# Performance work log

Hardware: AMD Instinct MI355X
Metric: run time of the kernel (lower is better)

Reference implementation:

```python
import jax, jax.numpy as jnp
import numpy as np

D = 1024
D_PRE_HEAD = 128
H = 16
D_ROPE = D_PRE_HEAD // 2          # 64
DC_V = D_PRE_HEAD                 # 128
DC_KV = D_PRE_HEAD // 8           # 16
DC_Q = D // 4                     # 256
Q_HEAD_DIM = D_PRE_HEAD + D_ROPE  # 192
MEG_D = D_PRE_HEAD + DC_V         # 256
MAX_LEN = 8192
EPS = 1e-7


def rms_norm(x, w):
    x32 = x.astype(jnp.float32)
    var = jnp.mean(x32 * x32, axis=-1, keepdims=True)
    return w * (x32 * jax.lax.rsqrt(var + EPS)).astype(x.dtype)


def rope_cos_sin():
    inv_freq = 1.0 / (10000.0 ** (jnp.arange(0, D_ROPE, 2, dtype=jnp.float32) / D_ROPE))
    freqs = jnp.outer(jnp.arange(MAX_LEN, dtype=jnp.float32), inv_freq)
    emb = jnp.concatenate([freqs, freqs], axis=-1)  # [MAX_LEN, D_ROPE]
    return jnp.cos(emb), jnp.sin(emb)


def rope_reshape(x):
    # view(...,d//2,2).transpose(-1,-2).reshape == concat(even, odd) along last dim
    return jnp.concatenate([x[..., 0::2], x[..., 1::2]], axis=-1)


def rope_rotate(x):
    h = x.shape[-1] // 2
    return jnp.concatenate([-x[..., h:], x[..., :h]], axis=-1)


def setup_inputs() -> dict:
    key = jax.random.key(0)
    ks = jax.random.split(key, 12)
    B, SQ, SKV = 2, 2048, 2048
    s = 0.02
    return {
        "q_inputs": jax.random.normal(ks[0], (B, SQ, D), jnp.float32),
        "kv_input": jax.random.normal(ks[1], (B, SKV, D), jnp.float32),
        "q_pos_ids": jax.random.randint(ks[2], (B, SQ), 0, MAX_LEN),
        "kv_pos_ids": jax.random.randint(ks[3], (B, SKV), 0, MAX_LEN),
        # weights stored as [in, out] (torch Linear weight transposed)
        "Wq_down": jax.random.normal(ks[4], (D, DC_Q), jnp.float32) * s,
        "q_norm_w": jnp.ones((DC_Q,), jnp.float32),
        "Wq_up": jax.random.normal(ks[5], (DC_Q, H * Q_HEAD_DIM), jnp.float32) * s,
        "Wkv_down": jax.random.normal(ks[6], (D, DC_KV + D_ROPE), jnp.float32) * s,
        "kv_norm_w": jnp.ones((DC_KV,), jnp.float32),
        "Wkv_up": jax.random.normal(ks[7], (DC_KV, H * MEG_D), jnp.float32) * s,
        "Wout": jax.random.normal(ks[8], (H * DC_V, D), jnp.float32) * s,
    }


def reference(q_inputs, kv_input, q_pos_ids, kv_pos_ids,
              Wq_down, q_norm_w, Wq_up, Wkv_down, kv_norm_w, Wkv_up, Wout):
    B, SQ, _ = q_inputs.shape
    SKV = kv_input.shape[1]

    # query path: low-rank down -> RMSNorm -> up
    q = rms_norm(q_inputs @ Wq_down, q_norm_w) @ Wq_up
    q = q.reshape(B, SQ, H, Q_HEAD_DIM).transpose(0, 2, 1, 3)  # [B,H,SQ,192]
    q_nope, q_rope = q[..., :D_PRE_HEAD], q[..., D_PRE_HEAD:]

    # kv path: compressed latent + decoupled rope slice
    ckv_full = kv_input @ Wkv_down                              # [B,SKV,DC_KV+D_ROPE]
    c_kv, k_rope = ckv_full[..., :DC_KV], ckv_full[..., DC_KV:]
    c_kv = rms_norm(c_kv, kv_norm_w)
    kv = (c_kv @ Wkv_up).reshape(B, SKV, H, MEG_D).transpose(0, 2, 1, 3)
    k_nope, value = kv[..., :D_PRE_HEAD], kv[..., D_PRE_HEAD:]  # [B,H,SKV,128] each
    k_rope = k_rope[:, None, :, :]                              # [B,1,SKV,64]

    # RoPE with per-token position ids
    cos, sin = rope_cos_sin()
    q_cos, q_sin = cos[q_pos_ids][:, None], sin[q_pos_ids][:, None]   # [B,1,SQ,64]
    k_cos, k_sin = cos[kv_pos_ids][:, None], sin[kv_pos_ids][:, None]
    qr = rope_reshape(q_rope)
    kr = rope_reshape(k_rope)
    q_rope = qr * q_cos + rope_rotate(qr) * q_sin
    k_rope = kr * k_cos + rope_rotate(kr) * k_sin

    query = jnp.concatenate([q_nope, q_rope], axis=-1)                         # [B,H,SQ,192]
    key_t = jnp.concatenate([k_nope, jnp.broadcast_to(k_rope, (B, H, SKV, D_ROPE))], axis=-1)

    scale = 1.0 / jnp.sqrt(jnp.asarray(Q_HEAD_DIM, query.dtype))
    scores = jnp.einsum('bhqd,bhkd->bhqk', query, key_t) * scale
    attn = jax.nn.softmax(scores, axis=-1)
    out = jnp.einsum('bhqk,bhkd->bhqd', attn, value)                           # [B,H,SQ,128]
    out = out.transpose(0, 2, 1, 3).reshape(B, SQ, H * DC_V)
    return out @ Wout
```

## Files before the change

### kernel.cpp

```cpp
#include <hip/hip_runtime.h>

typedef unsigned short u16;
typedef unsigned int u32;
typedef u16 u16x4 __attribute__((ext_vector_type(4)));
typedef u16 u16x8 __attribute__((ext_vector_type(8)));
typedef u32 u32x4 __attribute__((ext_vector_type(4)));
typedef float f32x4 __attribute__((ext_vector_type(4)));
typedef __bf16 bf16x8 __attribute__((ext_vector_type(8)));
typedef __bf16 bf16x2 __attribute__((ext_vector_type(2)));

#define DEV static __device__ __forceinline__

DEV float bf2f(u16 u) { u32 v = ((u32)u) << 16; float f; __builtin_memcpy(&f, &v, 4); return f; }
DEV u16 f2bf(float f) { u32 v; __builtin_memcpy(&v, &f, 4); v += 0x7fffu + ((v >> 16) & 1u); return (u16)(v >> 16); }
DEV bf16x8 ld_frag(const u16* p) { u16x8 v = *(const u16x8*)p; return __builtin_bit_cast(bf16x8, v); }

#define LOG10000 9.210340372f

__global__ __launch_bounds__(256) void k_wtrans5(
    const float* __restrict__ Wqd, const float* __restrict__ Wqu, const float* __restrict__ Wkvd,
    const float* __restrict__ Wkvu, const float* __restrict__ Wo,
    u16* __restrict__ WqdT, u16* __restrict__ WquT, u16* __restrict__ WkvdT,
    u16* __restrict__ WkvuT, u16* __restrict__ WoT) {
  __shared__ float tile[32][33];
  int id = blockIdx.x;
  const float* in; u16* out; int R, C, Rp, bx, by;
  if (id < 256)       { in = Wqd;  out = WqdT;  R = 1024; C = 256;  Rp = 1024; bx = id & 7;  by = id >> 3; }
  else if (id < 1024) { id -= 256;  in = Wqu;  out = WquT;  R = 256;  C = 3072; Rp = 256;  bx = id % 96; by = id / 96; }
  else if (id < 1152) { id -= 1024; in = Wkvd; out = WkvdT; R = 1024; C = 80;   Rp = 1024; bx = id & 3;  by = id >> 2; }
  else if (id < 1280) { id -= 1152; in = Wkvu; out = WkvuT; R = 16;   C = 4096; Rp = 32;   bx = id;      by = 0; }
  else                { id -= 1280; in = Wo;   out = WoT;   R = 2048; C = 1024; Rp = 2048; bx = id & 31; by = id >> 5; }
  int c0 = bx * 32, r0 = by * 32;
  int tx = threadIdx.x & 31, ty = threadIdx.x >> 5;
#pragma unroll
  for (int p = 0; p < 4; p++) {
    int r = r0 + ty + p * 8, c = c0 + tx;
    tile[ty + p * 8][tx] = (r < R && c < C) ? in[(size_t)r * C + c] : 0.f;
  }
  __syncthreads();
#pragma unroll
  for (int p = 0; p < 4; p++)
    out[(size_t)(c0 + ty + p * 8) * Rp + r0 + tx] = f2bf(tile[tx][ty + p * 8]);
}

DEV void gemm64f_body(int m0, int n0, const float* __restrict__ A, const u16* __restrict__ Bt,
                      float* __restrict__ C, int N, int K, int tid, u16* As, u16* Bs) {
  constexpr int LSTR = 40;
  const int l = tid & 63, w = tid >> 6;
  const int wr = (w >> 1) * 32, wc = (w & 1) * 32;
  const int lr = l & 15, lk = (l >> 4) * 8;
  const int sr = tid >> 2, sc = (tid & 3) * 8;
  f32x4 acc[2][2] = {};
  const float* pa0 = A + (size_t)(m0 + sr) * K + sc;
  const u16* pb0 = Bt + (size_t)(n0 + sr) * K + sc;
  f32x4 vaa = *(const f32x4*)pa0, vab = *(const f32x4*)(pa0 + 4);
  u16x8 vb0 = *(const u16x8*)pb0;
  for (int k0 = 0; k0 < K; k0 += 32) {
    u16x8 va0 = { f2bf(vaa[0]), f2bf(vaa[1]), f2bf(vaa[2]), f2bf(vaa[3]),
                  f2bf(vab[0]), f2bf(vab[1]), f2bf(vab[2]), f2bf(vab[3]) };
    *(u16x8*)&As[sr * LSTR + sc] = va0;
    *(u16x8*)&Bs[sr * LSTR + sc] = vb0;
    __syncthreads();
    if (k0 + 32 < K) {
      vaa = *(const f32x4*)(pa0 + k0 + 32);
      vab = *(const f32x4*)(pa0 + k0 + 36);
      vb0 = *(const u16x8*)(pb0 + k0 + 32);
    }
    bf16x8 af[2], bf[2];
#pragma unroll
    for (int i = 0; i < 2; i++) af[i] = ld_frag(&As[(wr + i * 16 + lr) * LSTR + lk]);
#pragma unroll
    for (int j = 0; j < 2; j++) bf[j] = ld_frag(&Bs[(wc + j * 16 + lr) * LSTR + lk]);
#pragma unroll
    for (int i = 0; i < 2; i++)
#pragma unroll
      for (int j = 0; j < 2; j++)
        acc[i][j] = __builtin_amdgcn_mfma_f32_16x16x32_bf16(af[i], bf[j], acc[i][j], 0, 0, 0);
    __syncthreads();
  }
#pragma unroll
  for (int i = 0; i < 2; i++)
#pragma unroll
    for (int j = 0; j < 2; j++) {
      int row = m0 + wr + i * 16 + (l >> 4) * 4;
      int col = n0 + wc + j * 16 + lr;
#pragma unroll
      for (int r = 0; r < 4; r++)
        C[(size_t)(row + r) * N + col] = acc[i][j][r];
    }
}

__global__ __launch_bounds__(256) void k_downs(const float* __restrict__ q_in, const float* __restrict__ kv_in,
                                               const u16* __restrict__ WqdT, const u16* __restrict__ WkvdT,
                                               float* __restrict__ cq, float* __restrict__ ckvf) {
  __shared__ u16 As[64 * 40], Bs[64 * 40];
  int id = blockIdx.x, tid = threadIdx.x;
  if (id < 128) {
    int swzb = (id & 7) * 16 + (id >> 3);
    gemm64f_body((swzb >> 1) * 64, (swzb & 1) * 64, kv_in, WkvdT, ckvf, 128, 1024, tid, As, Bs);
  } else {
    int lin = id - 128;
    int swzb = (lin & 7) * 32 + (lin >> 3);
    gemm64f_body((swzb >> 2) * 64, (swzb & 3) * 64, q_in, WqdT, cq, 256, 1024, tid, As, Bs);
  }
}

__global__ __launch_bounds__(256) void k_norms(const float* __restrict__ ckvf, const float* __restrict__ kvnw,
                                               const int* __restrict__ kpos, u16* __restrict__ ckvn,
                                               u16* __restrict__ kropeb,
                                               const float* __restrict__ cq, const float* __restrict__ qnw,
                                               u16* __restrict__ cqn, float scale) {
  int id = blockIdx.x, tid = threadIdx.x;
  int l = tid & 63;
  if (id < 1024) {
    int row = id * 4 + (tid >> 6);
    const float* x = ckvf + (size_t)row * 128;
    float v = (l < 16) ? x[l] : 0.f;
    float ss = v * v;
    ss += __shfl_xor(ss, 1); ss += __shfl_xor(ss, 2); ss += __shfl_xor(ss, 4); ss += __shfl_xor(ss, 8);
    if (l < 16) ckvn[(size_t)row * 32 + l] = f2bf(v * rsqrtf(ss * (1.f / 16.f) + 1e-7f) * kvnw[l]);
    if (l >= 16 && l < 32) ckvn[(size_t)row * 32 + l] = 0;
    if (l < 32) {
      float invf = __expf(-(LOG10000 / 32.f) * (float)l);
      float ang = (float)kpos[row] * invf;
      float c = cosf(ang), s = sinf(ang);
      float e = x[16 + 2 * l], o = x[17 + 2 * l];
      kropeb[(size_t)row * 64 + l]      = f2bf(e * c - o * s);
      kropeb[(size_t)row * 64 + l + 32] = f2bf(o * c + e * s);
    }
  } else {
    int row = (id - 1024) * 4 + (tid >> 6);
    const float* x = cq + (size_t)row * 256;
    f32x4 v = *(const f32x4*)(x + l * 4);
    float ss = v[0] * v[0] + v[1] * v[1] + v[2] * v[2] + v[3] * v[3];
#pragma unroll
    for (int m = 1; m < 64; m <<= 1) ss += __shfl_xor(ss, m);
    float rinv = rsqrtf(ss * (1.f / 256.f) + 1e-7f) * scale;
    const f32x4 wv = *(const f32x4*)(qnw + l * 4);
    u16x4 o = { f2bf(v[0] * rinv * wv[0]), f2bf(v[1] * rinv * wv[1]),
                f2bf(v[2] * rinv * wv[2]), f2bf(v[3] * rinv * wv[3]) };
    *(u16x4*)(cqn + (size_t)row * 256 + l * 4) = o;
  }
}

template <int MODE>
DEV void gemm128_body(int m0, int n0, const u16* __restrict__ A, const u16* __restrict__ Bt,
                      u16* __restrict__ C0, u16* __restrict__ C1, int N, int K, int tid,
                      u16* As, u16* Bs) {
  constexpr int LSTR = 40;
  const int l = tid & 63, w = tid >> 6;
  const int wr = (w >> 1) * 64, wc = (w & 1) * 64;
  const int lr = l & 15, lk = (l >> 4) * 8;
  const int sr = tid >> 2, sc = (tid & 3) * 8;
  f32x4 acc[4][4] = {};
  const u16* pa0 = A + (size_t)(m0 + sr) * K + sc;
  const u16* pa1 = A + (size_t)(m0 + 64 + sr) * K + sc;
  const u16* pb0 = Bt + (size_t)(n0 + sr) * K + sc;
  const u16* pb1 = Bt + (size_t)(n0 + 64 + sr) * K + sc;
  u16x8 va0 = *(const u16x8*)pa0, va1 = *(const u16x8*)pa1;
  u16x8 vb0 = *(const u16x8*)pb0, vb1 = *(const u16x8*)pb1;
  for (int k0 = 0; k0 < K; k0 += 32) {
    *(u16x8*)&As[sr * LSTR + sc] = va0;
    *(u16x8*)&As[(64 + sr) * LSTR + sc] = va1;
    *(u16x8*)&Bs[sr * LSTR + sc] = vb0;
    *(u16x8*)&Bs[(64 + sr) * LSTR + sc] = vb1;
    __syncthreads();
    if (k0 + 32 < K) {
      va0 = *(const u16x8*)(pa0 + k0 + 32);
      va1 = *(const u16x8*)(pa1 + k0 + 32);
      vb0 = *(const u16x8*)(pb0 + k0 + 32);
      vb1 = *(const u16x8*)(pb1 + k0 + 32);
    }
    bf16x8 af[4], bf[4];
#pragma unroll
    for (int i = 0; i < 4; i++) af[i] = ld_frag(&As[(wr + i * 16 + lr) * LSTR + lk]);
#pragma unroll
    for (int j = 0; j < 4; j++) bf[j] = ld_frag(&Bs[(wc + j * 16 + lr) * LSTR + lk]);
#pragma unroll
    for (int i = 0; i < 4; i++)
#pragma unroll
      for (int j = 0; j < 4; j++)
        acc[i][j] = __builtin_amdgcn_mfma_f32_16x16x32_bf16(af[i], bf[j], acc[i][j], 0, 0, 0);
    __syncthreads();
  }
  if (MODE == 0 || (n0 & 255) < 128) {
#pragma unroll
    for (int i = 0; i < 4; i++)
#pragma unroll
      for (int j = 0; j < 4; j++) {
        int row = m0 + wr + i * 16 + (l >> 4) * 4;
        int col = n0 + wc + j * 16 + lr;
#pragma unroll
        for (int r = 0; r < 4; r++)
          C0[(size_t)(row + r) * N + col] = f2bf(acc[i][j][r]);
      }
  } else {
#pragma unroll
    for (int i = 0; i < 4; i++)
#pragma unroll
      for (int j = 0; j < 4; j++) {
        int row = m0 + wr + i * 16 + (l >> 4) * 4;
        int col = n0 + wc + j * 16 + lr;
        int bb = row >> 11, srow = row & 2047;
        int hh2 = col >> 8, d = col & 127;
        u16x4 pk = { f2bf(acc[i][j][0]), f2bf(acc[i][j][1]),
                     f2bf(acc[i][j][2]), f2bf(acc[i][j][3]) };
        *(u16x4*)&C1[((size_t)(bb * 16 + hh2) * 128 + d) * 2048 + srow] = pk;
      }
  }
}

__global__ __launch_bounds__(256) void k_ups(const u16* __restrict__ ckvn, const u16* __restrict__ WkvuT,
                                             u16* __restrict__ Ckv, u16* __restrict__ VTb,
                                             const u16* __restrict__ cqn, const u16* __restrict__ WquT,
                                             u16* __restrict__ qproj) {
  __shared__ u16 As[128 * 40], Bs[128 * 40];
  int id = blockIdx.x, tid = threadIdx.x;
  if (id < 1024) {
    int swzb = (id & 7) * 128 + (id >> 3);
    gemm128_body<1>((swzb >> 5) * 128, (swzb & 31) * 128, ckvn, WkvuT, Ckv, VTb, 4096, 32, tid, As, Bs);
  } else {
    int lin = id - 1024;
    int swzb = (lin & 7) * 96 + (lin >> 3);
    gemm128_body<0>((swzb / 24) * 128, (swzb % 24) * 128, cqn, WquT, qproj, nullptr, 3072, 256, tid, As, Bs);
  }
}

__global__ __launch_bounds__(256) void k_gemmh(const u16* __restrict__ A, const u16* __restrict__ Bt,
                                               float* __restrict__ Cv, int M, int N, int K) {
  constexpr int LSTR = 40;
  __shared__ u16 As[64 * LSTR], Bs[128 * LSTR];
  const int tid = threadIdx.x, l = tid & 63, w = tid >> 6;
  const int nwg = gridDim.x * gridDim.y;
  const int lin = blockIdx.y * gridDim.x + blockIdx.x;
  const int swzb = (lin & 7) * (nwg >> 3) + (lin >> 3);
  const int m0 = (swzb / gridDim.x) * 64, n0 = (swzb % gridDim.x) * 128;
  const int wr = (w >> 1) * 32, wc = (w & 1) * 64;
  const int lr = l & 15, lk = (l >> 4) * 8;
  const int sr = tid >> 2, sc = (tid & 3) * 8;
  f32x4 acc[2][4] = {};
  const u16* pa0 = A + (size_t)(m0 + sr) * K + sc;
  const u16* pb0 = Bt + (size_t)(n0 + sr) * K + sc;
  const u16* pb1 = Bt + (size_t)(n0 + 64 + sr) * K + sc;
  u16x8 va0 = *(const u16x8*)pa0;
  u16x8 vb0 = *(const u16x8*)pb0, vb1 = *(const u16x8*)pb1;
  for (int k0 = 0; k0 < K; k0 += 32) {
    *(u16x8*)&As[sr * LSTR + sc] = va0;
    *(u16x8*)&Bs[sr * LSTR + sc] = vb0;
    *(u16x8*)&Bs[(64 + sr) * LSTR + sc] = vb1;
    __syncthreads();
    if (k0 + 32 < K) {
      va0 = *(const u16x8*)(pa0 + k0 + 32);
      vb0 = *(const u16x8*)(pb0 + k0 + 32);
      vb1 = *(const u16x8*)(pb1 + k0 + 32);
    }
    bf16x8 af[2], bf[4];
#pragma unroll
    for (int i = 0; i < 2; i++) af[i] = ld_frag(&As[(wr + i * 16 + lr) * LSTR + lk]);
#pragma unroll
    for (int j = 0; j < 4; j++) bf[j] = ld_frag(&Bs[(wc + j * 16 + lr) * LSTR + lk]);
#pragma unroll
    for (int i = 0; i < 2; i++)
#pragma unroll
      for (int j = 0; j < 4; j++)
        acc[i][j] = __builtin_amdgcn_mfma_f32_16x16x32_bf16(af[i], bf[j], acc[i][j], 0, 0, 0);
    __syncthreads();
  }
#pragma unroll
  for (int i = 0; i < 2; i++)
#pragma unroll
    for (int j = 0; j < 4; j++) {
      int row = m0 + wr + i * 16 + (l >> 4) * 4;
      int col = n0 + wc + j * 16 + lr;
#pragma unroll
      for (int r = 0; r < 4; r++)
        Cv[(size_t)(row + r) * N + col] = acc[i][j][r];
    }
}

__global__ __launch_bounds__(512, 2) void k_attn(const u16* __restrict__ Qp, const u16* __restrict__ Ckv,
                                                 const u16* __restrict__ kropeb, const u16* __restrict__ VT,
                                                 const int* __restrict__ qpos, u16* __restrict__ AO) {
  __shared__ u16 Ks[64 * 192];
  __shared__ u16 Vs[128 * 64];
  const int tid = threadIdx.x, l = tid & 63, w = tid >> 6;
  const int lr = l & 15, g = l >> 4, lk = g * 8;
  const int bid = blockIdx.x, bh = bid & 31, qt = bid >> 5;
  const int b = bh >> 4, hh = bh & 15;
  const int m0 = qt * 128;
  const u32 swz = (u32)(lr & 7) << 3;

  bf16x8 qa[6];
  {
    const int rowi = b * 2048 + m0 + w * 16 + lr;
    const u16* qrow = Qp + (size_t)rowi * 3072 + hh * 192;
#pragma unroll
    for (int kk = 0; kk < 4; kk++) qa[kk] = ld_frag(qrow + kk * 32 + lk);
    u16x8 e0 = *(const u16x8*)(qrow + 128 + 16 * g);
    u16x8 e1 = *(const u16x8*)(qrow + 136 + 16 * g);
    float fpos = (float)qpos[rowi];
    u16x8 r4, r5;
#pragma unroll
    for (int i = 0; i < 8; i++) {
      float invf = __expf(-(LOG10000 / 32.f) * (float)(8 * g + i));
      float ang = fpos * invf;
      float c = cosf(ang), s = sinf(ang);
      float ev = bf2f(i < 4 ? e0[2 * i] : e1[2 * i - 8]);
      float od = bf2f(i < 4 ? e0[2 * i + 1] : e1[2 * i - 7]);
      r4[i] = f2bf(ev * c - od * s);
      r5[i] = f2bf(od * c + ev * s);
    }
    qa[4] = __builtin_bit_cast(bf16x8, r4);
    qa[5] = __builtin_bit_cast(bf16x8, r5);
  }

  const u16* kptr[3]; int kstep[3]; u32 klds[3];
#pragma unroll
  for (int p = 0; p < 3; p++) {
    int c2 = tid + p * 512;
    int r = c2 / 24, cc = c2 - r * 24;
    klds[p] = (u32)(r * 192 + cc * 8) ^ ((u32)(r & 7) << 3);
    if (cc < 16) { kptr[p] = Ckv + ((size_t)(b * 2048 + r)) * 4096 + hh * 256 + cc * 8; kstep[p] = 64 * 4096; }
    else         { kptr[p] = kropeb + ((size_t)(b * 2048 + r)) * 64 + (cc - 16) * 8;    kstep[p] = 64 * 64; }
  }
  const u16* vptr[2]; u32 vlds[2];
#pragma unroll
  for (int p = 0; p < 2; p++) {
    int c2 = tid + p * 512;
    int d = c2 >> 3, cc = c2 & 7;
    vlds[p] = (u32)(d * 64 + cc * 8) ^ ((u32)(d & 7) << 3);
    vptr[p] = VT + ((size_t)bh * 128 + d) * 2048 + cc * 8;
  }
  u16x8 kreg[3], vreg[2];
#pragma unroll
  for (int p = 0; p < 3; p++) { kreg[p] = *(const u16x8*)kptr[p]; kptr[p] += kstep[p]; }
#pragma unroll
  for (int p = 0; p < 2; p++) { vreg[p] = *(const u16x8*)vptr[p]; vptr[p] += 64; }

  f32x4 oacc[8] = {};
  float lsum = 0.f;
  const int srcA = lr + ((l & 16) << 1);
  const int srcB = srcA + 16;
  const bool hi = (l & 32) != 0;

  for (int t = 0; t < 32; t++) {
#pragma unroll
    for (int p = 0; p < 3; p++) *(u16x8*)&Ks[klds[p]] = kreg[p];
#pragma unroll
    for (int p = 0; p < 2; p++) *(u16x8*)&Vs[vlds[p]] = vreg[p];
    __syncthreads();
    if (t + 1 < 32) {
#pragma unroll
      for (int p = 0; p < 3; p++) { kreg[p] = *(const u16x8*)kptr[p]; kptr[p] += kstep[p]; }
#pragma unroll
      for (int p = 0; p < 2; p++) { vreg[p] = *(const u16x8*)vptr[p]; vptr[p] += 64; }
    }
    f32x4 sacc[4] = {};
    __builtin_amdgcn_s_setprio(1);
#pragma unroll
    for (int n = 0; n < 4; n++)
#pragma unroll
      for (int kk = 0; kk < 6; kk++)
        sacc[n] = __builtin_amdgcn_mfma_f32_16x16x32_bf16(
            ld_frag(&Ks[(u32)((n * 16 + lr) * 192 + kk * 32 + lk) ^ swz]), qa[kk], sacc[n], 0, 0, 0);
    __builtin_amdgcn_s_setprio(0);
    u32 pw[4][2];
#pragma unroll
    for (int n = 0; n < 4; n++) {
      float p0 = __expf(sacc[n][0]), p1 = __expf(sacc[n][1]),
            p2 = __expf(sacc[n][2]), p3 = __expf(sacc[n][3]);
      lsum += (p0 + p1) + (p2 + p3);
      bf16x2 a01 = { (__bf16)p0, (__bf16)p1 };
      bf16x2 a23 = { (__bf16)p2, (__bf16)p3 };
      pw[n][0] = __builtin_bit_cast(u32, a01);
      pw[n][1] = __builtin_bit_cast(u32, a23);
    }
    u32 pa32[2][4];
#pragma unroll
    for (int kk2 = 0; kk2 < 2; kk2++) {
      u32 t0a = __shfl(pw[2 * kk2][0], srcA), t1a = __shfl(pw[2 * kk2 + 1][0], srcA);
      u32 t0b = __shfl(pw[2 * kk2][1], srcA), t1b = __shfl(pw[2 * kk2 + 1][1], srcA);
      u32 t0c = __shfl(pw[2 * kk2][0], srcB), t1c = __shfl(pw[2 * kk2 + 1][0], srcB);
      u32 t0d = __shfl(pw[2 * kk2][1], srcB), t1d = __shfl(pw[2 * kk2 + 1][1], srcB);
      pa32[kk2][0] = hi ? t1a : t0a;
      pa32[kk2][1] = hi ? t1b : t0b;
      pa32[kk2][2] = hi ? t1c : t0c;
      pa32[kk2][3] = hi ? t1d : t0d;
    }
    __builtin_amdgcn_s_setprio(1);
#pragma unroll
    for (int kk2 = 0; kk2 < 2; kk2++) {
      u32x4 pv = { pa32[kk2][0], pa32[kk2][1], pa32[kk2][2], pa32[kk2][3] };
      bf16x8 paf = __builtin_bit_cast(bf16x8, pv);
#pragma unroll
      for (int n2 = 0; n2 < 8; n2++)
        oacc[n2] = __builtin_amdgcn_mfma_f32_16x16x32_bf16(
            paf, ld_frag(&Vs[(u32)((n2 * 16 + lr) * 64 + kk2 * 32 + lk) ^ swz]), oacc[n2], 0, 0, 0);
    }
    __builtin_amdgcn_s_setprio(0);
    __syncthreads();
  }
  float s = lsum;
  s += __shfl_xor(s, 16);
  s += __shfl_xor(s, 32);
  float rl = 1.f / s;
  float rlv[4];
#pragma unroll
  for (int r = 0; r < 4; r++) rlv[r] = __shfl(rl, g * 4 + r);
#pragma unroll
  for (int n2 = 0; n2 < 8; n2++)
#pragma unroll
    for (int r = 0; r < 4; r++) {
      int row = m0 + w * 16 + g * 4 + r;
      AO[((size_t)(b * 2048 + row) * 16 + hh) * 128 + n2 * 16 + lr] = f2bf(oacc[n2][r] * rlv[r]);
    }
}

extern "C" void kernel_launch(void* const* d_in, const int* in_sizes, int n_in,
                              void* d_out, int out_size, void* d_ws, size_t ws_size,
                              hipStream_t stream) {
  const float* q_in  = (const float*)d_in[0];
  const float* kv_in = (const float*)d_in[1];
  const int*   qpos  = (const int*)d_in[2];
  const int*   kpos  = (const int*)d_in[3];
  const float* Wqd   = (const float*)d_in[4];
  const float* qnw   = (const float*)d_in[5];
  const float* Wqu   = (const float*)d_in[6];
  const float* Wkvd  = (const float*)d_in[7];
  const float* kvnw  = (const float*)d_in[8];
  const float* Wkvu  = (const float*)d_in[9];
  const float* Wo    = (const float*)d_in[10];
  float* out = (float*)d_out;
  char* ws = (char*)d_ws;
  size_t off = 0;
  auto alloc = [&](size_t bytes) -> void* {
    void* p = ws + off; off += (bytes + 255) & ~(size_t)255; return p;
  };
  u16*   WqdT   = (u16*)alloc(256ull * 1024 * 2);
  u16*   WquT   = (u16*)alloc(3072ull * 256 * 2);
  u16*   WkvdT  = (u16*)alloc(128ull * 1024 * 2);
  u16*   WkvuT  = (u16*)alloc(4096ull * 32 * 2);
  u16*   WoT    = (u16*)alloc(1024ull * 2048 * 2);
  float* ckvf   = (float*)alloc(4096ull * 128 * 4);
  u16*   ckvn   = (u16*)alloc(4096ull * 32 * 2);
  u16*   kropeb = (u16*)alloc(4096ull * 64 * 2);
  u16*   Ckv    = (u16*)alloc(4096ull * 4096 * 2);
  u16*   VTb    = (u16*)alloc(32ull * 128 * 2048 * 2);
  float* cq     = (float*)alloc(4096ull * 256 * 4);
  u16*   cqn    = (u16*)alloc(4096ull * 256 * 2);
  u16*   qproj  = (u16*)alloc(4096ull * 3072 * 2);
  u16*   AOb    = (u16*)alloc(4096ull * 2048 * 2);
  (void)in_sizes; (void)n_in; (void)out_size; (void)ws_size;

  k_wtrans5<<<3328, 256, 0, stream>>>(Wqd, Wqu, Wkvd, Wkvu, Wo, WqdT, WquT, WkvdT, WkvuT, WoT);
  k_downs<<<384, 256, 0, stream>>>(q_in, kv_in, WqdT, WkvdT, cq, ckvf);
  k_norms<<<2048, 256, 0, stream>>>(ckvf, kvnw, kpos, ckvn, kropeb, cq, qnw, cqn, 0.07216878364870322f);
  k_ups<<<1792, 256, 0, stream>>>(ckvn, WkvuT, Ckv, VTb, cqn, WquT, qproj);
  k_attn<<<512, 512, 0, stream>>>(qproj, Ckv, kropeb, VTb, qpos, AOb);
  k_gemmh<<<dim3(8, 64), 256, 0, stream>>>(AOb, WoT, out, 4096, 1024, 2048);
}
```

Before: 213.2 us.

## Double-buffer attention K/V tiles with direct global-to-LDS async loads

The attention kernel now loads K and V tiles straight from global memory into LDS with global_load_lds, instead of staging them through registers and then writing them to LDS. LDS is double-buffered so the next tile's load is issued while the current tile is being computed. The XOR swizzle moves from the LDS write address to the global read address, because each wave's lanes now write a contiguous LDS block. This removes the register staging and ds_write cost and one barrier per iteration, but doubles LDS per block, which could limit occupancy at two blocks per CU. It also relies on the compiler placing the right vmcnt waits before the barrier.

```diff
diff --git a/kernel.cpp b/kernel.cpp
--- a/kernel.cpp
+++ b/kernel.cpp
@@ -14,6 +14,10 @@
 DEV float bf2f(u16 u) { u32 v = ((u32)u) << 16; float f; __builtin_memcpy(&f, &v, 4); return f; }
 DEV u16 f2bf(float f) { u32 v; __builtin_memcpy(&v, &f, 4); v += 0x7fffu + ((v >> 16) & 1u); return (u16)(v >> 16); }
 DEV bf16x8 ld_frag(const u16* p) { u16x8 v = *(const u16x8*)p; return __builtin_bit_cast(bf16x8, v); }
+DEV void async_cp16(const u16* g, u16* l) {
+  __builtin_amdgcn_global_load_lds((const __attribute__((address_space(1))) void*)g,
+                                   (__attribute__((address_space(3))) void*)l, 16, 0, 0);
+}
 
 #define LOG10000 9.210340372f
 
@@ -281,8 +285,9 @@
 __global__ __launch_bounds__(512, 2) void k_attn(const u16* __restrict__ Qp, const u16* __restrict__ Ckv,
                                                  const u16* __restrict__ kropeb, const u16* __restrict__ VT,
                                                  const int* __restrict__ qpos, u16* __restrict__ AO) {
-  __shared__ u16 Ks[64 * 192];
-  __shared__ u16 Vs[128 * 64];
+  constexpr u32 KSZ = 64 * 192, VSZ = 128 * 64;
+  __shared__ u16 Ks[2 * KSZ];
+  __shared__ u16 Vs[2 * VSZ];
   const int tid = threadIdx.x, l = tid & 63, w = tid >> 6;
   const int lr = l & 15, g = l >> 4, lk = g * 8;
   const int bid = blockIdx.x, bh = bid & 31, qt = bid >> 5;
@@ -314,28 +319,30 @@
     qa[5] = __builtin_bit_cast(bf16x8, r5);
   }
 
-  const u16* kptr[3]; int kstep[3]; u32 klds[3];
+  const u16* kgp[3]; int kstp[3];
 #pragma unroll
   for (int p = 0; p < 3; p++) {
-    int c2 = tid + p * 512;
-    int r = c2 / 24, cc = c2 - r * 24;
-    klds[p] = (u32)(r * 192 + cc * 8) ^ ((u32)(r & 7) << 3);
-    if (cc < 16) { kptr[p] = Ckv + ((size_t)(b * 2048 + r)) * 4096 + hh * 256 + cc * 8; kstep[p] = 64 * 4096; }
-    else         { kptr[p] = kropeb + ((size_t)(b * 2048 + r)) * 64 + (cc - 16) * 8;    kstep[p] = 64 * 64; }
-  }
-  const u16* vptr[2]; u32 vlds[2];
+    int s = tid + p * 512;
+    int r = s / 24, c8 = s - r * 24;
+    int ccg = (c8 & ~7) | ((c8 & 7) ^ (r & 7));
+    if (ccg < 16) { kgp[p] = Ckv + ((size_t)(b * 2048 + r)) * 4096 + hh * 256 + ccg * 8; kstp[p] = 64 * 4096; }
+    else          { kgp[p] = kropeb + ((size_t)(b * 2048 + r)) * 64 + (ccg - 16) * 8;    kstp[p] = 64 * 64; }
+  }
+  const u16* vgp[2];
 #pragma unroll
   for (int p = 0; p < 2; p++) {
-    int c2 = tid + p * 512;
-    int d = c2 >> 3, cc = c2 & 7;
-    vlds[p] = (u32)(d * 64 + cc * 8) ^ ((u32)(d & 7) << 3);
-    vptr[p] = VT + ((size_t)bh * 128 + d) * 2048 + cc * 8;
-  }
-  u16x8 kreg[3], vreg[2];
-#pragma unroll
-  for (int p = 0; p < 3; p++) { kreg[p] = *(const u16x8*)kptr[p]; kptr[p] += kstep[p]; }
-#pragma unroll
-  for (int p = 0; p < 2; p++) { vreg[p] = *(const u16x8*)vptr[p]; vptr[p] += 64; }
+    int s = tid + p * 512;
+    int d = s >> 3, c8 = s & 7;
+    int ccg = c8 ^ (d & 7);
+    vgp[p] = VT + ((size_t)bh * 128 + d) * 2048 + ccg * 8;
+  }
+  const u32 wb = 512u * (u32)w;
+
+#pragma unroll
+  for (int p = 0; p < 3; p++) { async_cp16(kgp[p], &Ks[wb + 4096u * p]); kgp[p] += kstp[p]; }
+#pragma unroll
+  for (int p = 0; p < 2; p++) { async_cp16(vgp[p], &Vs[wb + 4096u * p]); vgp[p] += 64; }
+  __syncthreads();
 
   f32x4 oacc[8] = {};
   float lsum = 0.f;
@@ -344,17 +351,16 @@
   const bool hi = (l & 32) != 0;
 
   for (int t = 0; t < 32; t++) {
-#pragma unroll
-    for (int p = 0; p < 3; p++) *(u16x8*)&Ks[klds[p]] = kreg[p];
-#pragma unroll
-    for (int p = 0; p < 2; p++) *(u16x8*)&Vs[vlds[p]] = vreg[p];
-    __syncthreads();
+    const u32 cK = (u32)(t & 1) * KSZ, cV = (u32)(t & 1) * VSZ;
     if (t + 1 < 32) {
-#pragma unroll
-      for (int p = 0; p < 3; p++) { kreg[p] = *(const u16x8*)kptr[p]; kptr[p] += kstep[p]; }
-#pragma unroll
-      for (int p = 0; p < 2; p++) { vreg[p] = *(const u16x8*)vptr[p]; vptr[p] += 64; }
-    }
+      const u32 nK = cK ^ KSZ, nV = cV ^ VSZ;
+#pragma unroll
+      for (int p = 0; p < 3; p++) { async_cp16(kgp[p], &Ks[nK + wb + 4096u * p]); kgp[p] += kstp[p]; }
+#pragma unroll
+      for (int p = 0; p < 2; p++) { async_cp16(vgp[p], &Vs[nV + wb + 4096u * p]); vgp[p] += 64; }
+    }
+    const u16* KsC = &Ks[cK];
+    const u16* VsC = &Vs[cV];
     f32x4 sacc[4] = {};
     __builtin_amdgcn_s_setprio(1);
 #pragma unroll
@@ -362,7 +368,7 @@
 #pragma unroll
       for (int kk = 0; kk < 6; kk++)
         sacc[n] = __builtin_amdgcn_mfma_f32_16x16x32_bf16(
-            ld_frag(&Ks[(u32)((n * 16 + lr) * 192 + kk * 32 + lk) ^ swz]), qa[kk], sacc[n], 0, 0, 0);
+            ld_frag(&KsC[(u32)((n * 16 + lr) * 192 + kk * 32 + lk) ^ swz]), qa[kk], sacc[n], 0, 0, 0);
     __builtin_amdgcn_s_setprio(0);
     u32 pw[4][2];
 #pragma unroll
@@ -395,7 +401,7 @@
 #pragma unroll
       for (int n2 = 0; n2 < 8; n2++)
         oacc[n2] = __builtin_amdgcn_mfma_f32_16x16x32_bf16(
-            paf, ld_frag(&Vs[(u32)((n2 * 16 + lr) * 64 + kk2 * 32 + lk) ^ swz]), oacc[n2], 0, 0, 0);
+            paf, ld_frag(&VsC[(u32)((n2 * 16 + lr) * 64 + kk2 * 32 + lk) ^ swz]), oacc[n2], 0, 0, 0);
     }
     __builtin_amdgcn_s_setprio(0);
     __syncthreads();
```

New measurement: 216.6 us. No clear change (+1.6%).
